# Performance work log

Measured on AMD Instinct MI355X. Metric: run time of the kernel, lower is better.

## Reference

```python
import jax, jax.numpy as jnp
import numpy as np
from jax import lax

B, T, S, D = 16, 16, 196, 768
H = 256          # hidden_dim
NH = 4           # attention heads
TH = 32          # temporal hidden = max(16, H//8)
UP = 4           # UPSAMPLE_FACTOR


def _ln(x, w, b):
    m = jnp.mean(x, -1, keepdims=True)
    v = jnp.mean((x - m) ** 2, -1, keepdims=True)
    return (x - m) / jnp.sqrt(v + 1e-5) * w + b


def _gelu(x):
    return jax.nn.gelu(x, approximate=False)  # torch nn.GELU default (erf)


def _upmat(g, f):
    # torch F.interpolate bilinear, align_corners=False, as a [g*f, g] matrix
    g_up = g * f
    src = np.maximum((np.arange(g_up) + 0.5) / f - 0.5, 0.0)
    i0 = np.minimum(np.floor(src).astype(np.int64), g - 1)
    i1 = np.minimum(i0 + 1, g - 1)
    w1 = (src - i0).astype(np.float32)
    w0 = 1.0 - w1
    W = np.zeros((g_up, g), dtype=np.float32)
    np.add.at(W, (np.arange(g_up), i0), w0)
    np.add.at(W, (np.arange(g_up), i1), w1)
    return jnp.asarray(W)


def setup_inputs() -> dict:
    key = jax.random.key(0)
    ks = jax.random.split(key, 12)
    r = lambda i, shape: jax.random.normal(ks[i], shape, jnp.float32) * 0.02
    return dict(
        tokens=jax.random.normal(ks[0], (B, T * S, D), jnp.float32),
        num_frames=T,
        fixed_box_wh=jax.random.uniform(ks[1], (2,), jnp.float32, 0.1, 0.5),
        ln_w=jnp.ones((D,), jnp.float32), ln_b=jnp.zeros((D,), jnp.float32),
        query=r(2, (1, 1, D)),
        in_proj_w=r(3, (3 * D, D)), in_proj_b=jnp.zeros((3 * D,), jnp.float32),
        out_w=r(4, (D, D)), out_b=jnp.zeros((D,), jnp.float32),
        an_w=jnp.ones((D,), jnp.float32), an_b=jnp.zeros((D,), jnp.float32),
        obj_w=r(5, (1, D)), obj_b=jnp.zeros((1,), jnp.float32),
        temperature=jnp.asarray(8.0, jnp.float32),
        r1_w=r(6, (H, 2 * D)), r1_b=jnp.zeros((H,), jnp.float32),
        r2_w=r(7, (H // 2, H)), r2_b=jnp.zeros((H // 2,), jnp.float32),
        r3_w=r(8, (2, H // 2)), r3_b=jnp.zeros((2,), jnp.float32),
        tc1_w=r(9, (TH, 2, 5)), tc1_b=jnp.zeros((TH,), jnp.float32),
        tc2_w=r(10, (2, TH, 5)), tc2_b=jnp.zeros((2,), jnp.float32),
    )


def reference(tokens, num_frames, fixed_box_wh, ln_w, ln_b, query,
              in_proj_w, in_proj_b, out_w, out_b, an_w, an_b, obj_w, obj_b,
              temperature, r1_w, r1_b, r2_w, r2_b, r3_w, r3_b,
              tc1_w, tc1_b, tc2_w, tc2_b):
    Bb, N, Dd = tokens.shape
    Tt = int(num_frames)
    Ss = N // Tt
    g = int(round(Ss ** 0.5))
    g_up = g * UP
    BT = Bb * Tt
    dt = tokens.dtype

    normed = _ln(tokens, ln_w, ln_b)
    flat = normed.reshape(BT, Ss, Dd)  # per-frame tokens

    # --- attention pooling with learned query (dropout off, eval) ---
    Wq, Wk, Wv = jnp.split(in_proj_w, 3, 0)
    bq, bk, bv = jnp.split(in_proj_b, 3, 0)
    dh = Dd // NH
    qh = (query.reshape(1, Dd) @ Wq.T + bq).reshape(NH, dh)  # same query for all frames
    kh = (flat @ Wk.T + bk).reshape(BT, Ss, NH, dh)
    vh = (flat @ Wv.T + bv).reshape(BT, Ss, NH, dh)
    scores = jnp.einsum('hd,bshd->bhs', qh, kh) / jnp.sqrt(jnp.asarray(dh, dt))
    attnp = jax.nn.softmax(scores, -1)
    ctx = jnp.einsum('bhs,bshd->bhd', attnp, vh).reshape(BT, Dd)
    pooled = _ln(ctx @ out_w.T + out_b, an_w, an_b)

    obj = (flat @ obj_w.T + obj_b)[..., 0]  # [BT,S]
    Wu = _upmat(g, UP)
    up = jnp.einsum('ug,bgh,vh->buv', Wu, obj.reshape(BT, g, g), Wu)
    up = up.reshape(BT, g_up * g_up)
    temp = jnp.maximum(temperature, 1.0)
    probs = jax.nn.softmax(up * temp, -1)
    coords = (jnp.arange(g_up, dtype=dt) + 0.5) / g_up
    yy, xx = jnp.meshgrid(coords, coords, indexing='ij')
    cx0 = probs @ xx.reshape(-1)
    cy0 = probs @ yy.reshape(-1)

    # --- 3x3 local token gather around coarse center ---
    cxg = jnp.clip(cx0 * g, 0, g - 1).astype(jnp.int32)
    cyg = jnp.clip(cy0 * g, 0, g - 1).astype(jnp.int32)
    off = jnp.array([-1, 0, 1], jnp.int32)
    gy = jnp.clip(cyg[:, None, None] + off[None, :, None], 0, g - 1)
    gx = jnp.clip(cxg[:, None, None] + off[None, None, :], 0, g - 1)
    idx = (gy * g + gx).reshape(BT, 9)
    local = jnp.take_along_axis(flat, idx[:, :, None], axis=1).mean(1)

    # --- refine MLP ---
    h1 = _gelu(jnp.concatenate([pooled, local], -1) @ r1_w.T + r1_b)
    h2 = _gelu(h1 @ r2_w.T + r2_b)
    delta = h2 @ r3_w.T + r3_b
    cx = jnp.clip(cx0 + 0.3 * jnp.tanh(delta[:, 0]), 0.0, 1.0)
    cy = jnp.clip(cy0 + 0.3 * jnp.tanh(delta[:, 1]), 0.0, 1.0)

    # --- temporal residual refiner over center trajectories ---
    seq = jnp.stack([cx, cy], 1).reshape(Bb, Tt, 2).transpose(0, 2, 1)  # [B,2,T]
    dn = ('NCH', 'OIH', 'NCH')
    t1 = _gelu(lax.conv_general_dilated(seq, tc1_w, (1,), [(2, 2)],
                                        dimension_numbers=dn) + tc1_b[None, :, None])
    td = lax.conv_general_dilated(t1, tc2_w, (1,), [(2, 2)],
                                  dimension_numbers=dn) + tc2_b[None, :, None]
    td = td.transpose(0, 2, 1).reshape(BT, 2)
    cx = jnp.clip(cx + 0.12 * jnp.tanh(td[:, 0]), 0.0, 1.0)
    cy = jnp.clip(cy + 0.12 * jnp.tanh(td[:, 1]), 0.0, 1.0)

    # --- fixed-size boxes ---
    min_size = 1.0 / g
    wh = jnp.clip(jnp.broadcast_to(fixed_box_wh.reshape(1, 2), (Bb, 2)), min_size, 1.0)
    wh = jnp.broadcast_to(wh[:, None, :], (Bb, Tt, 2)).reshape(BT, 2)
    w, h = wh[:, 0], wh[:, 1]
    x1 = jnp.clip(cx - 0.5 * w, 0.0, 1.0)
    y1 = jnp.clip(cy - 0.5 * h, 0.0, 1.0)
    x2 = jnp.clip(cx + 0.5 * w, 0.0, 1.0)
    y2 = jnp.clip(cy + 0.5 * h, 0.0, 1.0)
    x2 = jnp.clip(jnp.maximum(x2, x1 + min_size), 0.0, 1.0)
    y2 = jnp.clip(jnp.maximum(y2, y1 + min_size), 0.0, 1.0)
    return jnp.stack([x1, y1, x2, y2], 1).reshape(Bb, Tt, 4)
```

## Files before the change

kernel.cpp:

```cpp
#include <hip/hip_runtime.h>
#include <hip/hip_bf16.h>
#include <math.h>

#define SS 196
#define DD 768

__device__ __forceinline__ float b2f(ushort u){
  union { unsigned int i; float f; } v; v.i = ((unsigned int)u) << 16; return v.f;
}
__device__ __forceinline__ bool bfmode(const void* lnw){
  return ((const ushort*)lnw)[0] != 0;
}
__device__ __forceinline__ float ldx(const void* p, size_t i, bool bf){
  return bf ? b2f(((const ushort*)p)[i]) : ((const float*)p)[i];
}
__device__ __forceinline__ float gelu_f(float x){
  return 0.5f * x * (1.0f + erff(x * 0.70710678118654752f));
}
__device__ __forceinline__ float wredsum(float v){
  #pragma unroll
  for(int o=32;o;o>>=1) v += __shfl_xor(v,o,64);
  return v;
}
__device__ __forceinline__ float wredmax(float v){
  #pragma unroll
  for(int o=32;o;o>>=1) v = fmaxf(v, __shfl_xor(v,o,64));
  return v;
}

__global__ __launch_bounds__(256) void k_qh(const void* __restrict__ q,
                                            const void* __restrict__ wq,
                                            const void* __restrict__ bq,
                                            const void* __restrict__ flagp,
                                            float* __restrict__ qh){
  bool bf = bfmode(flagp);
  int wv = threadIdx.x >> 6, lane = threadIdx.x & 63;
  int c = blockIdx.x * 4 + wv;
  float acc = 0.f;
  #pragma unroll
  for(int i=0;i<12;i++){ int d = lane + 64*i; acc += ldx(q,d,bf) * ldx(wq,(size_t)c*DD+d,bf); }
  acc = wredsum(acc);
  if(lane==0) qh[c] = acc + ldx(bq,c,bf);
}

__global__ __launch_bounds__(256) void k_wkpart(const void* __restrict__ wproj,
                                                const float* __restrict__ qh,
                                                const void* __restrict__ flagp,
                                                float* __restrict__ wkp){
  bool bf = bfmode(flagp);
  int idx = blockIdx.x*256 + threadIdx.x;
  int h = idx / DD, d = idx - h*DD;
  int c = blockIdx.y;
  const float* qp = qh + h*192 + c*12;
  size_t base = ((size_t)(DD + h*192 + c*12))*DD + d;
  float acc = 0.f;
  #pragma unroll
  for(int j=0;j<12;j++) acc += qp[j] * ldx(wproj, base + (size_t)j*DD, bf);
  wkp[(size_t)c*3072 + idx] = acc;
}

__global__ __launch_bounds__(256) void k_wkcomb(const float* __restrict__ wkp,
                                                const void* __restrict__ lnw,
                                                const void* __restrict__ objw,
                                                float* __restrict__ wkraw,
                                                float* __restrict__ wf){
  bool bf = bfmode(lnw);
  int idx = blockIdx.x*256 + threadIdx.x;
  int h = idx / DD, d = idx - h*DD;
  float s = 0.f;
  #pragma unroll
  for(int c=0;c<16;c++) s += wkp[(size_t)c*3072 + idx];
  wkraw[idx] = s;
  float w = ldx(lnw,d,bf);
  wf[idx] = w * s;
  if(h==0) wf[4*DD + d] = w * ldx(objw,d,bf);
}

__global__ __launch_bounds__(256) void k_consts(const float* __restrict__ wf,
                                                const float* __restrict__ wkraw,
                                                const void* __restrict__ lnb,
                                                const void* __restrict__ objw,
                                                const void* __restrict__ flagp,
                                                float* __restrict__ s12){
  bool bf = bfmode(flagp);
  int wv = threadIdx.x >> 6, lane = threadIdx.x & 63;
  for(int r = wv; r < 10; r += 4){
    float acc = 0.f;
    #pragma unroll
    for(int i=0;i<12;i++){
      int d = lane + 64*i;
      if(r < 5)      acc += wf[r*DD + d];
      else if(r < 9) acc += ldx(lnb,d,bf) * wkraw[(r-5)*DD + d];
      else           acc += ldx(lnb,d,bf) * ldx(objw,d,bf);
    }
    acc = wredsum(acc);
    if(lane==0) s12[r] = acc;
  }
}

__global__ __launch_bounds__(256) void k_pass1(const void* __restrict__ tok,
                                               const float* __restrict__ wf,
                                               const float* __restrict__ s12,
                                               const void* __restrict__ objb,
                                               const void* __restrict__ flagp,
                                               float* __restrict__ scores,
                                               float* __restrict__ objv,
                                               float* __restrict__ meanv,
                                               float* __restrict__ rstdv){
  __shared__ __align__(16) float swf[5*DD];
  __shared__ float ss12[10];
  for(int i=threadIdx.x;i<5*DD;i+=256) swf[i]=wf[i];
  if(threadIdx.x<10) ss12[threadIdx.x]=s12[threadIdx.x];
  __syncthreads();
  bool bf = bfmode(flagp);
  int wv = threadIdx.x >> 6, lane = threadIdx.x & 63;
  for(int it=0; it<4; it++){
    int tkn = blockIdx.x*16 + wv*4 + it;
    int f = tkn / SS, s = tkn - f*SS;
    float a0=0,a1=0,a2=0,a3=0,a4=0,sm=0,sq=0;
    if(bf){
      const ushort* x = (const ushort*)tok + (size_t)tkn * DD;
      #pragma unroll
      for(int i=0;i<3;i++){
        int d = 4*lane + 256*i;
        ushort4 u = *(const ushort4*)(x + d);
        float x0=b2f(u.x), x1=b2f(u.y), x2=b2f(u.z), x3=b2f(u.w);
        sm += (x0+x1)+(x2+x3); sq += (x0*x0+x1*x1)+(x2*x2+x3*x3);
        float4 w;
        w = *(const float4*)&swf[0*DD+d]; a0 += x0*w.x + x1*w.y + x2*w.z + x3*w.w;
        w = *(const float4*)&swf[1*DD+d]; a1 += x0*w.x + x1*w.y + x2*w.z + x3*w.w;
        w = *(const float4*)&swf[2*DD+d]; a2 += x0*w.x + x1*w.y + x2*w.z + x3*w.w;
        w = *(const float4*)&swf[3*DD+d]; a3 += x0*w.x + x1*w.y + x2*w.z + x3*w.w;
        w = *(const float4*)&swf[4*DD+d]; a4 += x0*w.x + x1*w.y + x2*w.z + x3*w.w;
      }
    } else {
      const float* x = (const float*)tok + (size_t)tkn * DD;
      #pragma unroll
      for(int i=0;i<3;i++){
        int d = 4*lane + 256*i;
        float4 u = *(const float4*)(x + d);
        sm += u.x+u.y+u.z+u.w;
        sq += u.x*u.x+u.y*u.y+u.z*u.z+u.w*u.w;
        float4 w;
        w = *(const float4*)&swf[0*DD+d]; a0 += u.x*w.x+u.y*w.y+u.z*w.z+u.w*w.w;
        w = *(const float4*)&swf[1*DD+d]; a1 += u.x*w.x+u.y*w.y+u.z*w.z+u.w*w.w;
        w = *(const float4*)&swf[2*DD+d]; a2 += u.x*w.x+u.y*w.y+u.z*w.z+u.w*w.w;
        w = *(const float4*)&swf[3*DD+d]; a3 += u.x*w.x+u.y*w.y+u.z*w.z+u.w*w.w;
        w = *(const float4*)&swf[4*DD+d]; a4 += u.x*w.x+u.y*w.y+u.z*w.z+u.w*w.w;
      }
    }
    sm=wredsum(sm); sq=wredsum(sq);
    a0=wredsum(a0); a1=wredsum(a1); a2=wredsum(a2); a3=wredsum(a3); a4=wredsum(a4);
    if(lane==0){
      const float invD = 1.0f/768.0f;
      float m = sm*invD;
      float var = sq*invD - m*m;
      float rstd = rsqrtf(var + 1e-5f);
      meanv[tkn]=m; rstdv[tkn]=rstd;
      const float sc = 0.07216878364870322f;
      scores[(f*4+0)*SS+s] = (rstd*(a0 - m*ss12[0]) + ss12[5]) * sc;
      scores[(f*4+1)*SS+s] = (rstd*(a1 - m*ss12[1]) + ss12[6]) * sc;
      scores[(f*4+2)*SS+s] = (rstd*(a2 - m*ss12[2]) + ss12[7]) * sc;
      scores[(f*4+3)*SS+s] = (rstd*(a3 - m*ss12[3]) + ss12[8]) * sc;
      objv[tkn] = rstd*(a4 - m*ss12[4]) + ss12[9] + ldx(objb,0,bf);
    }
  }
}

__global__ __launch_bounds__(512) void k_softobj(const void* __restrict__ tok,
                                                 float* __restrict__ aw,
                                                 const float* __restrict__ objv,
                                                 const float* __restrict__ meanv,
                                                 const float* __restrict__ rstdv,
                                                 const void* __restrict__ temp,
                                                 const void* __restrict__ lnw,
                                                 const void* __restrict__ lnb,
                                                 float* __restrict__ pl,
                                                 float* __restrict__ cterm,
                                                 float* __restrict__ cxy){
  bool bf = bfmode(lnw);
  int f = blockIdx.x, tid = threadIdx.x;
  int wv = tid >> 6, lane = tid & 63;
  __shared__ float sobj[196];
  __shared__ float up[3136];
  __shared__ int   i0a[56], i1a[56];
  __shared__ float w0a[56], w1a[56];
  __shared__ float redm[4], reds[8], redx[8], redy[8];
  __shared__ int   sidx[9];
  __shared__ float rj[9], rmj[9];
  if(tid<196) sobj[tid] = objv[(size_t)f*SS + tid];
  if(tid<56){
    float src = fmaxf((tid+0.5f)*0.25f - 0.5f, 0.0f);
    int i0 = min((int)floorf(src), 13);
    i0a[tid]=i0; i1a[tid]=min(i0+1,13);
    float w1 = src - (float)i0;
    w1a[tid]=w1; w0a[tid]=1.0f-w1;
  }
  __syncthreads();
  if(wv < 4){
    int h = wv;
    float* sc = aw + (size_t)(f*4+h)*SS;
    const float* rs = rstdv + f*SS;
    const float* mv = meanv + f*SS;
    float v[4]; float mx = -1e30f;
    #pragma unroll
    for(int j=0;j<4;j++){ int s=lane+64*j; v[j] = (s<SS)? sc[s] : -1e30f; mx=fmaxf(mx,v[j]); }
    mx = wredmax(mx);
    float e[4], sum=0.f;
    #pragma unroll
    for(int j=0;j<4;j++){ int s=lane+64*j; e[j] = (s<SS)? expf(v[j]-mx) : 0.f; sum += e[j]; }
    sum = wredsum(sum);
    float inv = 1.0f/sum;
    float cp = 0.f;
    #pragma unroll
    for(int j=0;j<4;j++){
      int s=lane+64*j;
      if(s<SS){ float r=rs[s]; float a=e[j]*inv*r; sc[s]=a; cp += a*mv[s]; }
    }
    cp = wredsum(cp);
    if(lane==0) cterm[f*4+h] = cp;
  } else {
    int w4 = wv-4;
    float lmax = -1e30f;
    for(int i = w4*64 + lane; i<3136; i+=256){
      int u=i/56, v=i-u*56;
      float val = w0a[u]*(w0a[v]*sobj[i0a[u]*14+i0a[v]] + w1a[v]*sobj[i0a[u]*14+i1a[v]])
                + w1a[u]*(w0a[v]*sobj[i1a[u]*14+i0a[v]] + w1a[v]*sobj[i1a[u]*14+i1a[v]]);
      up[i]=val; lmax=fmaxf(lmax,val);
    }
    lmax = wredmax(lmax);
    if(lane==0) redm[w4]=lmax;
  }
  __syncthreads();
  float mx = fmaxf(fmaxf(redm[0],redm[1]), fmaxf(redm[2],redm[3]));
  float t = fmaxf(ldx(temp,0,bf), 1.0f);
  float se=0, sx=0, sy=0;
  for(int i=tid;i<3136;i+=512){
    int u=i/56, v=i-u*56;
    float e = expf((up[i]-mx)*t);
    se += e;
    sx += e * ((v+0.5f)*(1.0f/56.0f));
    sy += e * ((u+0.5f)*(1.0f/56.0f));
  }
  se=wredsum(se); sx=wredsum(sx); sy=wredsum(sy);
  if(lane==0){ reds[wv]=se; redx[wv]=sx; redy[wv]=sy; }
  __syncthreads();
  se=0; sx=0; sy=0;
  #pragma unroll
  for(int i=0;i<8;i++){ se+=reds[i]; sx+=redx[i]; sy+=redy[i]; }
  float cx0 = sx/se, cy0 = sy/se;
  if(tid==0){ cxy[f*2]=cx0; cxy[f*2+1]=cy0; }
  float vx = fminf(fmaxf(cx0*14.0f,0.0f),13.0f); int cxg=(int)vx;
  float vy = fminf(fmaxf(cy0*14.0f,0.0f),13.0f); int cyg=(int)vy;
  if(tid<9){
    int dy = tid/3 - 1, dx = tid%3 - 1;
    int gy = min(max(cyg+dy,0),13), gx = min(max(cxg+dx,0),13);
    int s = gy*14+gx;
    sidx[tid]=s;
    float r = rstdv[(size_t)f*SS+s];
    rj[tid]=r; rmj[tid]=r*meanv[(size_t)f*SS+s];
  }
  __syncthreads();
  float offc = 0.f;
  #pragma unroll
  for(int j=0;j<9;j++) offc += rmj[j];
  for(int d=tid; d<DD; d+=512){
    float acc = 0.f;
    #pragma unroll
    for(int j=0;j<9;j++) acc += rj[j]*ldx(tok, (size_t)f*SS*DD + (size_t)sidx[j]*DD + d, bf);
    pl[(size_t)f*1536 + DD + d] = ldx(lnw,d,bf)*((acc-offc)*(1.0f/9.0f)) + ldx(lnb,d,bf);
  }
}

__global__ __launch_bounds__(256) void k_xbar_part(const void* __restrict__ tok,
                                                   const float* __restrict__ aw,
                                                   const void* __restrict__ flagp,
                                                   float* __restrict__ xpart){
  bool bf = bfmode(flagp);
  int f = blockIdx.x, c = blockIdx.y;
  __shared__ float a4[49*4];
  for(int i=threadIdx.x;i<49*4;i+=256){
    int s=i>>2, h=i&3;
    a4[i]=aw[(size_t)(f*4+h)*SS + c*49 + s];
  }
  __syncthreads();
  float acc[3][4] = {};
  if(bf){
    const ushort* tf = (const ushort*)tok + (size_t)(f*SS + c*49)*DD;
    #pragma unroll 7
    for(int s=0;s<49;s++){
      float w0=a4[s*4+0], w1=a4[s*4+1], w2=a4[s*4+2], w3=a4[s*4+3];
      #pragma unroll
      for(int j=0;j<3;j++){
        float x = b2f(tf[(size_t)s*DD + threadIdx.x + 256*j]);
        acc[j][0]+=w0*x; acc[j][1]+=w1*x; acc[j][2]+=w2*x; acc[j][3]+=w3*x;
      }
    }
  } else {
    const float* tf = (const float*)tok + (size_t)(f*SS + c*49)*DD;
    #pragma unroll 7
    for(int s=0;s<49;s++){
      float w0=a4[s*4+0], w1=a4[s*4+1], w2=a4[s*4+2], w3=a4[s*4+3];
      #pragma unroll
      for(int j=0;j<3;j++){
        float x = tf[(size_t)s*DD + threadIdx.x + 256*j];
        acc[j][0]+=w0*x; acc[j][1]+=w1*x; acc[j][2]+=w2*x; acc[j][3]+=w3*x;
      }
    }
  }
  #pragma unroll
  for(int j=0;j<3;j++){
    int d = threadIdx.x + 256*j;
    size_t base = (((size_t)c*256 + f)*4)*DD + d;
    xpart[base + 0*DD] = acc[j][0];
    xpart[base + 1*DD] = acc[j][1];
    xpart[base + 2*DD] = acc[j][2];
    xpart[base + 3*DD] = acc[j][3];
  }
}

__global__ __launch_bounds__(256) void k_xbar_comb(const float* __restrict__ xpart,
                                                   const float* __restrict__ cterm,
                                                   const void* __restrict__ lnw,
                                                   const void* __restrict__ lnb,
                                                   float* __restrict__ xbar){
  bool bf = bfmode(lnw);
  int f = blockIdx.x;
  float c0=cterm[f*4+0], c1=cterm[f*4+1], c2=cterm[f*4+2], c3=cterm[f*4+3];
  #pragma unroll
  for(int j=0;j<3;j++){
    int d = threadIdx.x + 256*j;
    float w=ldx(lnw,d,bf), b=ldx(lnb,d,bf);
    float s0=0,s1=0,s2=0,s3=0;
    #pragma unroll
    for(int c=0;c<4;c++){
      size_t base = (((size_t)c*256 + f)*4)*DD + d;
      s0 += xpart[base + 0*DD];
      s1 += xpart[base + 1*DD];
      s2 += xpart[base + 2*DD];
      s3 += xpart[base + 3*DD];
    }
    xbar[((size_t)(f*4+0))*DD+d] = w*(s0-c0)+b;
    xbar[((size_t)(f*4+1))*DD+d] = w*(s1-c1)+b;
    xbar[((size_t)(f*4+2))*DD+d] = w*(s2-c2)+b;
    xbar[((size_t)(f*4+3))*DD+d] = w*(s3-c3)+b;
  }
}

template<int N, int K, int ACT, int CTX, int ROWOFF>
__global__ __launch_bounds__(256) void k_tgemm(const float* __restrict__ A,
                                               const void* __restrict__ W,
                                               const void* __restrict__ bias,
                                               const void* __restrict__ flagp,
                                               float* __restrict__ C){
  bool bf = bfmode(flagp);
  __shared__ float As[32][32];
  __shared__ float Bs[32][64];
  int tid = threadIdx.x;
  int n0 = blockIdx.x*64, m0 = blockIdx.y*32;
  int h  = n0 / 192;
  int am = tid>>3, ak = (tid&7)*4;
  int bn = tid>>2, bk = (tid&3)*8;
  const float* ap = A + (CTX ? ((size_t)((m0+am)*4+h))*768 : (size_t)(m0+am)*K) + ak;
  const ushort* wpb = (const ushort*)W + (size_t)(ROWOFF+n0+bn)*K + bk;
  const float*  wpf = (const float*)W  + (size_t)(ROWOFF+n0+bn)*K + bk;
  int tx = tid&15, ty = tid>>4;
  float acc[2][4] = {};
  float4 av; float b8[8];
  av = *(const float4*)ap;
  if(bf){
    ushort4 w0 = *(const ushort4*)(wpb);
    ushort4 w1 = *(const ushort4*)(wpb+4);
    b8[0]=b2f(w0.x); b8[1]=b2f(w0.y); b8[2]=b2f(w0.z); b8[3]=b2f(w0.w);
    b8[4]=b2f(w1.x); b8[5]=b2f(w1.y); b8[6]=b2f(w1.z); b8[7]=b2f(w1.w);
  } else {
    float4 w0 = *(const float4*)(wpf);
    float4 w1 = *(const float4*)(wpf+4);
    b8[0]=w0.x; b8[1]=w0.y; b8[2]=w0.z; b8[3]=w0.w;
    b8[4]=w1.x; b8[5]=w1.y; b8[6]=w1.z; b8[7]=w1.w;
  }
  for(int k0=0; k0<K; k0+=32){
    As[ak+0][am]=av.x; As[ak+1][am]=av.y; As[ak+2][am]=av.z; As[ak+3][am]=av.w;
    #pragma unroll
    for(int j=0;j<8;j++) Bs[bk+j][bn]=b8[j];
    __syncthreads();
    float4 av2; float b82[8];
    if(k0+32 < K){
      av2 = *(const float4*)(ap + k0 + 32);
      if(bf){
        ushort4 w0 = *(const ushort4*)(wpb + k0 + 32);
        ushort4 w1 = *(const ushort4*)(wpb + k0 + 36);
        b82[0]=b2f(w0.x); b82[1]=b2f(w0.y); b82[2]=b2f(w0.z); b82[3]=b2f(w0.w);
        b82[4]=b2f(w1.x); b82[5]=b2f(w1.y); b82[6]=b2f(w1.z); b82[7]=b2f(w1.w);
      } else {
        float4 w0 = *(const float4*)(wpf + k0 + 32);
        float4 w1 = *(const float4*)(wpf + k0 + 36);
        b82[0]=w0.x; b82[1]=w0.y; b82[2]=w0.z; b82[3]=w0.w;
        b82[4]=w1.x; b82[5]=w1.y; b82[6]=w1.z; b82[7]=w1.w;
      }
    }
    #pragma unroll
    for(int k=0;k<32;k++){
      float2 a = *(const float2*)&As[k][ty*2];
      float4 b = *(const float4*)&Bs[k][tx*4];
      acc[0][0]+=a.x*b.x; acc[0][1]+=a.x*b.y; acc[0][2]+=a.x*b.z; acc[0][3]+=a.x*b.w;
      acc[1][0]+=a.y*b.x; acc[1][1]+=a.y*b.y; acc[1][2]+=a.y*b.z; acc[1][3]+=a.y*b.w;
    }
    __syncthreads();
    av = av2;
    #pragma unroll
    for(int j=0;j<8;j++) b8[j]=b82[j];
  }
  int n = n0 + tx*4;
  float bv0=ldx(bias,ROWOFF+n,bf),   bv1=ldx(bias,ROWOFF+n+1,bf),
        bv2=ldx(bias,ROWOFF+n+2,bf), bv3=ldx(bias,ROWOFF+n+3,bf);
  #pragma unroll
  for(int i=0;i<2;i++){
    int m = m0 + ty*2 + i;
    float4 o;
    o.x=acc[i][0]+bv0; o.y=acc[i][1]+bv1; o.z=acc[i][2]+bv2; o.w=acc[i][3]+bv3;
    if(ACT){ o.x=gelu_f(o.x); o.y=gelu_f(o.y); o.z=gelu_f(o.z); o.w=gelu_f(o.w); }
    *(float4*)&C[(size_t)m*N + n] = o;
  }
}

__global__ __launch_bounds__(256) void k_lnan(const float* __restrict__ X,
                                              const void* __restrict__ anw,
                                              const void* __restrict__ anb,
                                              const void* __restrict__ flagp,
                                              float* __restrict__ pl){
  bool bf = bfmode(flagp);
  int wv = threadIdx.x >> 6, lane = threadIdx.x & 63;
  int f = blockIdx.x*4 + wv;
  const float* x = X + (size_t)f*DD;
  float v[12]; float sm=0, sq=0;
  #pragma unroll
  for(int i=0;i<12;i++){ v[i]=x[lane+64*i]; sm+=v[i]; sq+=v[i]*v[i]; }
  sm=wredsum(sm); sq=wredsum(sq);
  float m = sm*(1.0f/768.0f);
  float rstd = rsqrtf(sq*(1.0f/768.0f) - m*m + 1e-5f);
  #pragma unroll
  for(int i=0;i<12;i++){
    int d = lane+64*i;
    pl[(size_t)f*1536 + d] = (v[i]-m)*rstd*ldx(anw,d,bf) + ldx(anb,d,bf);
  }
}

__global__ __launch_bounds__(256) void k_final(const float* __restrict__ h2,
                                               const void* __restrict__ r3w,
                                               const void* __restrict__ r3b,
                                               const float* __restrict__ cxy,
                                               const void* __restrict__ tc1w,
                                               const void* __restrict__ tc1b,
                                               const void* __restrict__ tc2w,
                                               const void* __restrict__ tc2b,
                                               const void* __restrict__ fbw,
                                               const void* __restrict__ flagp,
                                               void* __restrict__ out){
  bool bf = bfmode(flagp);
  __shared__ float sxs[256], sys[256];
  __shared__ float t1[16*32*16];
  __shared__ float td[16*2*16];
  int f = threadIdx.x;
  float a0=0.f, a1=0.f;
  const float* hh = h2 + (size_t)f*128;
  for(int k=0;k<128;k++){ float x=hh[k]; a0 += x*ldx(r3w,k,bf); a1 += x*ldx(r3w,128+k,bf); }
  a0 += ldx(r3b,0,bf); a1 += ldx(r3b,1,bf);
  float cx1 = fminf(fmaxf(cxy[f*2]   + 0.3f*tanhf(a0), 0.f), 1.f);
  float cy1 = fminf(fmaxf(cxy[f*2+1] + 0.3f*tanhf(a1), 0.f), 1.f);
  sxs[f]=cx1; sys[f]=cy1;
  __syncthreads();
  for(int idx=f; idx<8192; idx+=256){
    int b = idx>>9, o = (idx>>4)&31, t = idx&15;
    float acc = ldx(tc1b,o,bf);
    #pragma unroll
    for(int k=0;k<5;k++){
      int tt = t + k - 2;
      if(tt>=0 && tt<16)
        acc += sxs[b*16+tt]*ldx(tc1w,o*10 + k,bf) + sys[b*16+tt]*ldx(tc1w,o*10 + 5 + k,bf);
    }
    t1[idx] = gelu_f(acc);
  }
  __syncthreads();
  for(int idx=f; idx<512; idx+=256){
    int b = idx>>5, c = (idx>>4)&1, t = idx&15;
    float acc = ldx(tc2b,c,bf);
    for(int o=0;o<32;o++){
      #pragma unroll
      for(int k=0;k<5;k++){
        int tt = t + k - 2;
        if(tt>=0 && tt<16) acc += t1[(b*32+o)*16+tt]*ldx(tc2w,(c*32+o)*5+k,bf);
      }
    }
    td[(b*2+c)*16+t] = acc;
  }
  __syncthreads();
  {
    int b = f>>4;
    float tdx = td[(b*2+0)*16+(f&15)], tdy = td[(b*2+1)*16+(f&15)];
    float cx2 = fminf(fmaxf(sxs[f] + 0.12f*tanhf(tdx), 0.f), 1.f);
    float cy2 = fminf(fmaxf(sys[f] + 0.12f*tanhf(tdy), 0.f), 1.f);
    const float ms = 1.0f/14.0f;
    float w  = fminf(fmaxf(ldx(fbw,0,bf), ms), 1.f);
    float ht = fminf(fmaxf(ldx(fbw,1,bf), ms), 1.f);
    float x1 = fminf(fmaxf(cx2 - 0.5f*w , 0.f), 1.f);
    float y1 = fminf(fmaxf(cy2 - 0.5f*ht, 0.f), 1.f);
    float x2 = fminf(fmaxf(cx2 + 0.5f*w , 0.f), 1.f);
    float y2 = fminf(fmaxf(cy2 + 0.5f*ht, 0.f), 1.f);
    x2 = fminf(fmaxf(fmaxf(x2, x1+ms), 0.f), 1.f);
    y2 = fminf(fmaxf(fmaxf(y2, y1+ms), 0.f), 1.f);
    if(bf){
      __hip_bfloat16* ob = (__hip_bfloat16*)out;
      ob[f*4+0]=__float2bfloat16(x1);
      ob[f*4+1]=__float2bfloat16(y1);
      ob[f*4+2]=__float2bfloat16(x2);
      ob[f*4+3]=__float2bfloat16(y2);
    } else {
      float* of = (float*)out;
      of[f*4+0]=x1; of[f*4+1]=y1; of[f*4+2]=x2; of[f*4+3]=y2;
    }
  }
}

extern "C" void kernel_launch(void* const* d_in, const int* in_sizes, int n_in,
                              void* d_out, int out_size, void* d_ws, size_t ws_size,
                              hipStream_t stream){
  (void)in_sizes; (void)n_in; (void)out_size; (void)ws_size;
  const void* tok   = d_in[0];
  const void* fbw   = d_in[2];
  const void* lnw   = d_in[3];
  const void* lnb   = d_in[4];
  const void* query = d_in[5];
  const void* wproj = d_in[6];
  const void* bproj = d_in[7];
  const void* outw  = d_in[8];
  const void* outb  = d_in[9];
  const void* anw   = d_in[10];
  const void* anb   = d_in[11];
  const void* objw  = d_in[12];
  const void* objb  = d_in[13];
  const void* temp  = d_in[14];
  const void* r1w   = d_in[15];
  const void* r1b   = d_in[16];
  const void* r2w   = d_in[17];
  const void* r2b   = d_in[18];
  const void* r3w   = d_in[19];
  const void* r3b   = d_in[20];
  const void* tc1w  = d_in[21];
  const void* tc1b  = d_in[22];
  const void* tc2w  = d_in[23];
  const void* tc2b  = d_in[24];

  float* ws    = (float*)d_ws;
  float* qh    = ws;
  float* wkraw = ws + 768;
  float* wf    = wkraw + 3072;
  float* s12   = wf + 3840;
  float* wkp   = s12 + 16;
  float* scores= wkp + 49152;
  float* objv  = scores + 200704;
  float* meanv = objv + 50176;
  float* rstdv = meanv + 50176;
  float* cterm = rstdv + 50176;
  float* xbar  = cterm + 1024;
  float* ctx   = xbar + 786432;
  float* ppre  = ctx + 196608;
  float* pl    = ppre + 196608;
  float* h1    = pl + 393216;
  float* h2    = h1 + 65536;
  float* cxy   = h2 + 32768;
  float* xpart = cxy + 512;

  hipLaunchKernelGGL(k_qh,     dim3(192),    dim3(256), 0, stream, query, wproj, bproj, lnw, qh);
  hipLaunchKernelGGL(k_wkpart, dim3(12,16),  dim3(256), 0, stream, wproj, qh, lnw, wkp);
  hipLaunchKernelGGL(k_wkcomb, dim3(12),     dim3(256), 0, stream, wkp, lnw, objw, wkraw, wf);
  hipLaunchKernelGGL(k_consts, dim3(1),      dim3(256), 0, stream, wf, wkraw, lnb, objw, lnw, s12);
  hipLaunchKernelGGL(k_pass1,  dim3(3136),   dim3(256), 0, stream, tok, wf, s12, objb, lnw, scores, objv, meanv, rstdv);
  hipLaunchKernelGGL(k_softobj,dim3(256),    dim3(512), 0, stream, tok, scores, objv, meanv, rstdv, temp, lnw, lnb, pl, cterm, cxy);
  hipLaunchKernelGGL(k_xbar_part, dim3(256,4), dim3(256), 0, stream, tok, scores, lnw, xpart);
  hipLaunchKernelGGL(k_xbar_comb, dim3(256),   dim3(256), 0, stream, xpart, cterm, lnw, lnb, xbar);
  hipLaunchKernelGGL((k_tgemm<768,768,0,1,1536>), dim3(12,8), dim3(256), 0, stream, xbar, wproj, bproj, lnw, ctx);
  hipLaunchKernelGGL((k_tgemm<768,768,0,0,0>),    dim3(12,8), dim3(256), 0, stream, ctx, outw, outb, lnw, ppre);
  hipLaunchKernelGGL(k_lnan,   dim3(64),     dim3(256), 0, stream, ppre, anw, anb, lnw, pl);
  hipLaunchKernelGGL((k_tgemm<256,1536,1,0,0>), dim3(4,8), dim3(256), 0, stream, pl, r1w, r1b, lnw, h1);
  hipLaunchKernelGGL((k_tgemm<128,256,1,0,0>),  dim3(2,8), dim3(256), 0, stream, h1, r2w, r2b, lnw, h2);
  hipLaunchKernelGGL(k_final,  dim3(1),      dim3(256), 0, stream, h2, r3w, r3b, cxy, tc1w, tc1b, tc2w, tc2b, fbw, lnw, (void*)d_out);
}
```

Baseline: 519.6 us.

## Fuse tiny setup kernels and re-map pass1 and xbar_part thread work

Folds the query projection into k_wkpart, with each block computing its 12 needed q values in shared memory. It also folds the k_consts reduction into k_wkcomb as per-block partial sums that k_pass1 adds up at load time, which removes two launches. k_pass1 now assigns 16 threads per token instead of a whole wave, with a shorter shuffle reduction. k_xbar_part uses 192 threads doing vectorized 4-wide loads and stores instead of 256 threads doing scalar accesses. The risks are redundant q computation across blocks and idle threads in xbar_part.

```diff
diff --git a/kernel.cpp b/kernel.cpp
--- a/kernel.cpp
+++ b/kernel.cpp
@@ -28,79 +28,86 @@
   return v;
 }
 
-__global__ __launch_bounds__(256) void k_qh(const void* __restrict__ q,
-                                            const void* __restrict__ wq,
-                                            const void* __restrict__ bq,
-                                            const void* __restrict__ flagp,
-                                            float* __restrict__ qh){
-  bool bf = bfmode(flagp);
-  int wv = threadIdx.x >> 6, lane = threadIdx.x & 63;
-  int c = blockIdx.x * 4 + wv;
-  float acc = 0.f;
-  #pragma unroll
-  for(int i=0;i<12;i++){ int d = lane + 64*i; acc += ldx(q,d,bf) * ldx(wq,(size_t)c*DD+d,bf); }
-  acc = wredsum(acc);
-  if(lane==0) qh[c] = acc + ldx(bq,c,bf);
-}
-
 __global__ __launch_bounds__(256) void k_wkpart(const void* __restrict__ wproj,
-                                                const float* __restrict__ qh,
+                                                const void* __restrict__ query,
+                                                const void* __restrict__ bproj,
                                                 const void* __restrict__ flagp,
                                                 float* __restrict__ wkp){
   bool bf = bfmode(flagp);
-  int idx = blockIdx.x*256 + threadIdx.x;
-  int h = idx / DD, d = idx - h*DD;
-  int c = blockIdx.y;
-  const float* qp = qh + h*192 + c*12;
+  int bx = blockIdx.x, c = blockIdx.y;
+  int tid = threadIdx.x;
+  int wv = tid>>6, lane = tid&63;
+  int h = bx/3;
+  __shared__ float sqh[12];
+  #pragma unroll
+  for(int j = wv*3; j < wv*3+3; j++){
+    int rr = h*192 + c*12 + j;
+    float acc = 0.f;
+    #pragma unroll
+    for(int i=0;i<12;i++){ int d = lane + 64*i; acc += ldx(query,d,bf) * ldx(wproj,(size_t)rr*DD+d,bf); }
+    acc = wredsum(acc);
+    if(lane==0) sqh[j] = acc + ldx(bproj, rr, bf);
+  }
+  __syncthreads();
+  int idx = bx*256 + tid;
+  int d = idx - h*DD;
   size_t base = ((size_t)(DD + h*192 + c*12))*DD + d;
   float acc = 0.f;
   #pragma unroll
-  for(int j=0;j<12;j++) acc += qp[j] * ldx(wproj, base + (size_t)j*DD, bf);
+  for(int j=0;j<12;j++) acc += sqh[j] * ldx(wproj, base + (size_t)j*DD, bf);
   wkp[(size_t)c*3072 + idx] = acc;
 }
 
 __global__ __launch_bounds__(256) void k_wkcomb(const float* __restrict__ wkp,
                                                 const void* __restrict__ lnw,
+                                                const void* __restrict__ lnb,
                                                 const void* __restrict__ objw,
                                                 float* __restrict__ wkraw,
-                                                float* __restrict__ wf){
+                                                float* __restrict__ wf,
+                                                float* __restrict__ s12p){
   bool bf = bfmode(lnw);
-  int idx = blockIdx.x*256 + threadIdx.x;
+  int bx = blockIdx.x;
+  int idx = bx*256 + threadIdx.x;
   int h = idx / DD, d = idx - h*DD;
   float s = 0.f;
   #pragma unroll
   for(int c=0;c<16;c++) s += wkp[(size_t)c*3072 + idx];
   wkraw[idx] = s;
   float w = ldx(lnw,d,bf);
-  wf[idx] = w * s;
-  if(h==0) wf[4*DD + d] = w * ldx(objw,d,bf);
-}
-
-__global__ __launch_bounds__(256) void k_consts(const float* __restrict__ wf,
-                                                const float* __restrict__ wkraw,
-                                                const void* __restrict__ lnb,
-                                                const void* __restrict__ objw,
-                                                const void* __restrict__ flagp,
-                                                float* __restrict__ s12){
-  bool bf = bfmode(flagp);
-  int wv = threadIdx.x >> 6, lane = threadIdx.x & 63;
-  for(int r = wv; r < 10; r += 4){
-    float acc = 0.f;
-    #pragma unroll
-    for(int i=0;i<12;i++){
-      int d = lane + 64*i;
-      if(r < 5)      acc += wf[r*DD + d];
-      else if(r < 9) acc += ldx(lnb,d,bf) * wkraw[(r-5)*DD + d];
-      else           acc += ldx(lnb,d,bf) * ldx(objw,d,bf);
-    }
-    acc = wredsum(acc);
-    if(lane==0) s12[r] = acc;
+  float wfv = w * s;
+  wf[idx] = wfv;
+  float lb = ldx(lnb,d,bf);
+  float p0 = wfv;
+  float p5 = lb * s;
+  float p4 = 0.f, p9 = 0.f;
+  if(bx < 3){
+    float ow = ldx(objw,d,bf);
+    float wfo = w * ow;
+    wf[4*DD + d] = wfo;
+    p4 = wfo;
+    p9 = lb * ow;
+  }
+  p0 = wredsum(p0); p5 = wredsum(p5); p4 = wredsum(p4); p9 = wredsum(p9);
+  __shared__ float red[4][4];
+  int wv = threadIdx.x>>6, lane = threadIdx.x&63;
+  if(lane==0){ red[0][wv]=p0; red[1][wv]=p5; red[2][wv]=p4; red[3][wv]=p9; }
+  __syncthreads();
+  if(threadIdx.x==0){
+    float q0=red[0][0]+red[0][1]+red[0][2]+red[0][3];
+    float q5=red[1][0]+red[1][1]+red[1][2]+red[1][3];
+    float q4=red[2][0]+red[2][1]+red[2][2]+red[2][3];
+    float q9=red[3][0]+red[3][1]+red[3][2]+red[3][3];
+    #pragma unroll
+    for(int r=0;r<10;r++) s12p[bx*10+r]=0.f;
+    s12p[bx*10 + h] = q0;
+    s12p[bx*10 + 5 + h] = q5;
+    if(bx<3){ s12p[bx*10 + 4] = q4; s12p[bx*10 + 9] = q9; }
   }
 }
 
 __global__ __launch_bounds__(256) void k_pass1(const void* __restrict__ tok,
                                                const float* __restrict__ wf,
-                                               const float* __restrict__ s12,
+                                               const float* __restrict__ s12p,
                                                const void* __restrict__ objb,
                                                const void* __restrict__ flagp,
                                                float* __restrict__ scores,
@@ -110,60 +117,69 @@
   __shared__ __align__(16) float swf[5*DD];
   __shared__ float ss12[10];
   for(int i=threadIdx.x;i<5*DD;i+=256) swf[i]=wf[i];
-  if(threadIdx.x<10) ss12[threadIdx.x]=s12[threadIdx.x];
+  if(threadIdx.x<10){
+    float a=0.f;
+    #pragma unroll
+    for(int b=0;b<12;b++) a += s12p[b*10+threadIdx.x];
+    ss12[threadIdx.x]=a;
+  }
   __syncthreads();
   bool bf = bfmode(flagp);
-  int wv = threadIdx.x >> 6, lane = threadIdx.x & 63;
-  for(int it=0; it<4; it++){
-    int tkn = blockIdx.x*16 + wv*4 + it;
-    int f = tkn / SS, s = tkn - f*SS;
-    float a0=0,a1=0,a2=0,a3=0,a4=0,sm=0,sq=0;
-    if(bf){
-      const ushort* x = (const ushort*)tok + (size_t)tkn * DD;
-      #pragma unroll
-      for(int i=0;i<3;i++){
-        int d = 4*lane + 256*i;
-        ushort4 u = *(const ushort4*)(x + d);
-        float x0=b2f(u.x), x1=b2f(u.y), x2=b2f(u.z), x3=b2f(u.w);
-        sm += (x0+x1)+(x2+x3); sq += (x0*x0+x1*x1)+(x2*x2+x3*x3);
-        float4 w;
-        w = *(const float4*)&swf[0*DD+d]; a0 += x0*w.x + x1*w.y + x2*w.z + x3*w.w;
-        w = *(const float4*)&swf[1*DD+d]; a1 += x0*w.x + x1*w.y + x2*w.z + x3*w.w;
-        w = *(const float4*)&swf[2*DD+d]; a2 += x0*w.x + x1*w.y + x2*w.z + x3*w.w;
-        w = *(const float4*)&swf[3*DD+d]; a3 += x0*w.x + x1*w.y + x2*w.z + x3*w.w;
-        w = *(const float4*)&swf[4*DD+d]; a4 += x0*w.x + x1*w.y + x2*w.z + x3*w.w;
-      }
-    } else {
-      const float* x = (const float*)tok + (size_t)tkn * DD;
-      #pragma unroll
-      for(int i=0;i<3;i++){
-        int d = 4*lane + 256*i;
-        float4 u = *(const float4*)(x + d);
-        sm += u.x+u.y+u.z+u.w;
-        sq += u.x*u.x+u.y*u.y+u.z*u.z+u.w*u.w;
-        float4 w;
-        w = *(const float4*)&swf[0*DD+d]; a0 += u.x*w.x+u.y*w.y+u.z*w.z+u.w*w.w;
-        w = *(const float4*)&swf[1*DD+d]; a1 += u.x*w.x+u.y*w.y+u.z*w.z+u.w*w.w;
-        w = *(const float4*)&swf[2*DD+d]; a2 += u.x*w.x+u.y*w.y+u.z*w.z+u.w*w.w;
-        w = *(const float4*)&swf[3*DD+d]; a3 += u.x*w.x+u.y*w.y+u.z*w.z+u.w*w.w;
-        w = *(const float4*)&swf[4*DD+d]; a4 += u.x*w.x+u.y*w.y+u.z*w.z+u.w*w.w;
-      }
-    }
-    sm=wredsum(sm); sq=wredsum(sq);
-    a0=wredsum(a0); a1=wredsum(a1); a2=wredsum(a2); a3=wredsum(a3); a4=wredsum(a4);
-    if(lane==0){
-      const float invD = 1.0f/768.0f;
-      float m = sm*invD;
-      float var = sq*invD - m*m;
-      float rstd = rsqrtf(var + 1e-5f);
-      meanv[tkn]=m; rstdv[tkn]=rstd;
-      const float sc = 0.07216878364870322f;
-      scores[(f*4+0)*SS+s] = (rstd*(a0 - m*ss12[0]) + ss12[5]) * sc;
-      scores[(f*4+1)*SS+s] = (rstd*(a1 - m*ss12[1]) + ss12[6]) * sc;
-      scores[(f*4+2)*SS+s] = (rstd*(a2 - m*ss12[2]) + ss12[7]) * sc;
-      scores[(f*4+3)*SS+s] = (rstd*(a3 - m*ss12[3]) + ss12[8]) * sc;
-      objv[tkn] = rstd*(a4 - m*ss12[4]) + ss12[9] + ldx(objb,0,bf);
-    }
+  int tid = threadIdx.x;
+  int tl = tid & 15;
+  int tkn = blockIdx.x*16 + (tid>>4);
+  int f = tkn / SS, s = tkn - f*SS;
+  float a0=0,a1=0,a2=0,a3=0,a4=0,sm=0,sq=0;
+  if(bf){
+    const ushort* x = (const ushort*)tok + (size_t)tkn * DD;
+    #pragma unroll
+    for(int i=0;i<12;i++){
+      int d = 4*tl + 64*i;
+      ushort4 u = *(const ushort4*)(x + d);
+      float x0=b2f(u.x), x1=b2f(u.y), x2=b2f(u.z), x3=b2f(u.w);
+      sm += (x0+x1)+(x2+x3); sq += (x0*x0+x1*x1)+(x2*x2+x3*x3);
+      float4 w;
+      w = *(const float4*)&swf[0*DD+d]; a0 += x0*w.x + x1*w.y + x2*w.z + x3*w.w;
+      w = *(const float4*)&swf[1*DD+d]; a1 += x0*w.x + x1*w.y + x2*w.z + x3*w.w;
+      w = *(const float4*)&swf[2*DD+d]; a2 += x0*w.x + x1*w.y + x2*w.z + x3*w.w;
+      w = *(const float4*)&swf[3*DD+d]; a3 += x0*w.x + x1*w.y + x2*w.z + x3*w.w;
+      w = *(const float4*)&swf[4*DD+d]; a4 += x0*w.x + x1*w.y + x2*w.z + x3*w.w;
+    }
+  } else {
+    const float* x = (const float*)tok + (size_t)tkn * DD;
+    #pragma unroll
+    for(int i=0;i<12;i++){
+      int d = 4*tl + 64*i;
+      float4 u = *(const float4*)(x + d);
+      sm += (u.x+u.y)+(u.z+u.w);
+      sq += (u.x*u.x+u.y*u.y)+(u.z*u.z+u.w*u.w);
+      float4 w;
+      w = *(const float4*)&swf[0*DD+d]; a0 += u.x*w.x+u.y*w.y+u.z*w.z+u.w*w.w;
+      w = *(const float4*)&swf[1*DD+d]; a1 += u.x*w.x+u.y*w.y+u.z*w.z+u.w*w.w;
+      w = *(const float4*)&swf[2*DD+d]; a2 += u.x*w.x+u.y*w.y+u.z*w.z+u.w*w.w;
+      w = *(const float4*)&swf[3*DD+d]; a3 += u.x*w.x+u.y*w.y+u.z*w.z+u.w*w.w;
+      w = *(const float4*)&swf[4*DD+d]; a4 += u.x*w.x+u.y*w.y+u.z*w.z+u.w*w.w;
+    }
+  }
+  #pragma unroll
+  for(int o=8;o;o>>=1){
+    sm += __shfl_xor(sm,o,64); sq += __shfl_xor(sq,o,64);
+    a0 += __shfl_xor(a0,o,64); a1 += __shfl_xor(a1,o,64);
+    a2 += __shfl_xor(a2,o,64); a3 += __shfl_xor(a3,o,64);
+    a4 += __shfl_xor(a4,o,64);
+  }
+  if(tl==0){
+    const float invD = 1.0f/768.0f;
+    float m = sm*invD;
+    float var = sq*invD - m*m;
+    float rstd = rsqrtf(var + 1e-5f);
+    meanv[tkn]=m; rstdv[tkn]=rstd;
+    const float sc = 0.07216878364870322f;
+    scores[(f*4+0)*SS+s] = (rstd*(a0 - m*ss12[0]) + ss12[5]) * sc;
+    scores[(f*4+1)*SS+s] = (rstd*(a1 - m*ss12[1]) + ss12[6]) * sc;
+    scores[(f*4+2)*SS+s] = (rstd*(a2 - m*ss12[2]) + ss12[7]) * sc;
+    scores[(f*4+3)*SS+s] = (rstd*(a3 - m*ss12[3]) + ss12[8]) * sc;
+    objv[tkn] = rstd*(a4 - m*ss12[4]) + ss12[9] + ldx(objb,0,bf);
   }
 }
 
@@ -284,38 +300,39 @@
     a4[i]=aw[(size_t)(f*4+h)*SS + c*49 + s];
   }
   __syncthreads();
-  float acc[3][4] = {};
-  if(bf){
-    const ushort* tf = (const ushort*)tok + (size_t)(f*SS + c*49)*DD;
-    #pragma unroll 7
-    for(int s=0;s<49;s++){
-      float w0=a4[s*4+0], w1=a4[s*4+1], w2=a4[s*4+2], w3=a4[s*4+3];
-      #pragma unroll
-      for(int j=0;j<3;j++){
-        float x = b2f(tf[(size_t)s*DD + threadIdx.x + 256*j]);
-        acc[j][0]+=w0*x; acc[j][1]+=w1*x; acc[j][2]+=w2*x; acc[j][3]+=w3*x;
+  int tid = threadIdx.x;
+  if(tid < 192){
+    int d = tid*4;
+    float4 A0={0,0,0,0},A1={0,0,0,0},A2={0,0,0,0},A3={0,0,0,0};
+    if(bf){
+      const ushort* tf = (const ushort*)tok + (size_t)(f*SS + c*49)*DD + d;
+      #pragma unroll 7
+      for(int s=0;s<49;s++){
+        ushort4 u = *(const ushort4*)(tf + (size_t)s*DD);
+        float x0=b2f(u.x), x1=b2f(u.y), x2=b2f(u.z), x3=b2f(u.w);
+        float w0=a4[s*4+0], w1=a4[s*4+1], w2=a4[s*4+2], w3=a4[s*4+3];
+        A0.x+=w0*x0; A0.y+=w0*x1; A0.z+=w0*x2; A0.w+=w0*x3;
+        A1.x+=w1*x0; A1.y+=w1*x1; A1.z+=w1*x2; A1.w+=w1*x3;
+        A2.x+=w2*x0; A2.y+=w2*x1; A2.z+=w2*x2; A2.w+=w2*x3;
+        A3.x+=w3*x0; A3.y+=w3*x1; A3.z+=w3*x2; A3.w+=w3*x3;
       }
-    }
-  } else {
-    const float* tf = (const float*)tok + (size_t)(f*SS + c*49)*DD;
-    #pragma unroll 7
-    for(int s=0;s<49;s++){
-      float w0=a4[s*4+0], w1=a4[s*4+1], w2=a4[s*4+2], w3=a4[s*4+3];
-      #pragma unroll
-      for(int j=0;j<3;j++){
-        float x = tf[(size_t)s*DD + threadIdx.x + 256*j];
-        acc[j][0]+=w0*x; acc[j][1]+=w1*x; acc[j][2]+=w2*x; acc[j][3]+=w3*x;
+    } else {
+      const float* tf = (const float*)tok + (size_t)(f*SS + c*49)*DD + d;
+      #pragma unroll 7
+      for(int s=0;s<49;s++){
+        float4 u = *(const float4*)(tf + (size_t)s*DD);
+        float w0=a4[s*4+0], w1=a4[s*4+1], w2=a4[s*4+2], w3=a4[s*4+3];
+        A0.x+=w0*u.x; A0.y+=w0*u.y; A0.z+=w0*u.z; A0.w+=w0*u.w;
+        A1.x+=w1*u.x; A1.y+=w1*u.y; A1.z+=w1*u.z; A1.w+=w1*u.w;
+        A2.x+=w2*u.x; A2.y+=w2*u.y; A2.z+=w2*u.z; A2.w+=w2*u.w;
+        A3.x+=w3*u.x; A3.y+=w3*u.y; A3.z+=w3*u.z; A3.w+=w3*u.w;
       }
     }
-  }
-  #pragma unroll
-  for(int j=0;j<3;j++){
-    int d = threadIdx.x + 256*j;
     size_t base = (((size_t)c*256 + f)*4)*DD + d;
-    xpart[base + 0*DD] = acc[j][0];
-    xpart[base + 1*DD] = acc[j][1];
-    xpart[base + 2*DD] = acc[j][2];
-    xpart[base + 3*DD] = acc[j][3];
+    *(float4*)&xpart[base + 0*DD] = A0;
+    *(float4*)&xpart[base + 1*DD] = A1;
+    *(float4*)&xpart[base + 2*DD] = A2;
+    *(float4*)&xpart[base + 3*DD] = A3;
   }
 }
 
@@ -552,11 +569,10 @@
   const void* tc2b  = d_in[24];
 
   float* ws    = (float*)d_ws;
-  float* qh    = ws;
-  float* wkraw = ws + 768;
+  float* wkraw = ws;
   float* wf    = wkraw + 3072;
-  float* s12   = wf + 3840;
-  float* wkp   = s12 + 16;
+  float* s12p  = wf + 3840;
+  float* wkp   = s12p + 128;
   float* scores= wkp + 49152;
   float* objv  = scores + 200704;
   float* meanv = objv + 50176;
@@ -571,11 +587,9 @@
   float* cxy   = h2 + 32768;
   float* xpart = cxy + 512;
 
-  hipLaunchKernelGGL(k_qh,     dim3(192),    dim3(256), 0, stream, query, wproj, bproj, lnw, qh);
-  hipLaunchKernelGGL(k_wkpart, dim3(12,16),  dim3(256), 0, stream, wproj, qh, lnw, wkp);
-  hipLaunchKernelGGL(k_wkcomb, dim3(12),     dim3(256), 0, stream, wkp, lnw, objw, wkraw, wf);
-  hipLaunchKernelGGL(k_consts, dim3(1),      dim3(256), 0, stream, wf, wkraw, lnb, objw, lnw, s12);
-  hipLaunchKernelGGL(k_pass1,  dim3(3136),   dim3(256), 0, stream, tok, wf, s12, objb, lnw, scores, objv, meanv, rstdv);
+  hipLaunchKernelGGL(k_wkpart, dim3(12,16),  dim3(256), 0, stream, wproj, query, bproj, lnw, wkp);
+  hipLaunchKernelGGL(k_wkcomb, dim3(12),     dim3(256), 0, stream, wkp, lnw, lnb, objw, wkraw, wf, s12p);
+  hipLaunchKernelGGL(k_pass1,  dim3(3136),   dim3(256), 0, stream, tok, wf, s12p, objb, lnw, scores, objv, meanv, rstdv);
   hipLaunchKernelGGL(k_softobj,dim3(256),    dim3(512), 0, stream, tok, scores, objv, meanv, rstdv, temp, lnw, lnb, pl, cterm, cxy);
   hipLaunchKernelGGL(k_xbar_part, dim3(256,4), dim3(256), 0, stream, tok, scores, lnw, xpart);
   hipLaunchKernelGGL(k_xbar_comb, dim3(256),   dim3(256), 0, stream, xpart, cterm, lnw, lnb, xbar);
```

New measurement: 505.1 us, median of 2. 2.8% less time.
